# Kernel optimization log

Measured on AMD Instinct MI355X. Metric: run time of the kernel, lower is better.

The kernel has to match this reference:

```python
import jax, jax.numpy as jnp
import numpy as np

FREQ_MASK_PARAM = 20
TIME_MASK_PARAM = 40
NUM_FREQ_MASKS = 2
NUM_TIME_MASKS = 2
NOISE_STD = 0.01
P_APPLY = 0.5

B, C, F, T = 64, 2, 128, 2048


def setup_inputs() -> dict:
    key = jax.random.key(0)
    ks = jax.random.split(key, 7)
    return {
        "spec": jax.random.normal(ks[0], (B, C, F, T), dtype=jnp.float32),
        "apply_u": jax.random.uniform(ks[1], (B,), dtype=jnp.float32),
        "f_width_u": jax.random.uniform(ks[2], (B, NUM_FREQ_MASKS), dtype=jnp.float32),
        "f_start_u": jax.random.uniform(ks[3], (B, NUM_FREQ_MASKS), dtype=jnp.float32),
        "t_width_u": jax.random.uniform(ks[4], (B, NUM_TIME_MASKS), dtype=jnp.float32),
        "t_start_u": jax.random.uniform(ks[5], (B, NUM_TIME_MASKS), dtype=jnp.float32),
        "noise": jax.random.normal(ks[6], (B, C, F, T), dtype=jnp.float32),
    }


def _band_mask(width_u, start_u, size, max_param, clamp_min_one):
    # width = int(u * max_param); start = int(u * (size - width)) (optionally max(1, .))
    w = jnp.floor(width_u * max_param).astype(jnp.int32)          # [B, K]
    rng = (size - w).astype(jnp.float32)
    if clamp_min_one:
        rng = jnp.maximum(rng, 1.0)
    s0 = jnp.floor(start_u * rng).astype(jnp.int32)               # [B, K]
    idx = jnp.arange(size, dtype=jnp.int32)                       # [size]
    hit = (idx[None, None, :] >= s0[:, :, None]) & (idx[None, None, :] < (s0 + w)[:, :, None])
    return jnp.any(hit, axis=1)                                   # [B, size] True = zeroed


def reference(spec, apply_u, f_width_u, f_start_u, t_width_u, t_start_u, noise):
    b, c, f, t = spec.shape
    fmask = _band_mask(f_width_u, f_start_u, f, FREQ_MASK_PARAM, clamp_min_one=False)  # [B,F]
    tmask = _band_mask(t_width_u, t_start_u, t, TIME_MASK_PARAM, clamp_min_one=True)   # [B,T]
    keep = (~fmask)[:, None, :, None] & (~tmask)[:, None, None, :]                     # [B,1,F,T]
    aug = jnp.where(keep, spec, jnp.float32(0.0)) + noise * jnp.float32(NOISE_STD)
    apply = (apply_u <= P_APPLY)[:, None, None, None]
    return jnp.where(apply, aug, spec)
```

## Files before the change

kernel.cpp:

```cpp
#include <hip/hip_runtime.h>


#define BB 64
#define CC 2
#define FF 128
#define TT 2048

__global__ __launch_bounds__(256) void specaug_kernel(
    const float* __restrict__ spec,
    const float* __restrict__ apply_u,
    const float* __restrict__ f_width_u,
    const float* __restrict__ f_start_u,
    const float* __restrict__ t_width_u,
    const float* __restrict__ t_start_u,
    const float* __restrict__ noise,
    float* __restrict__ out)
{
    const int vec = blockIdx.x * blockDim.x + threadIdx.x;
    const int tv  = vec & (TT / 4 - 1);
    const int row = vec >> 9;
    const int f   = row & (FF - 1);
    const int b   = row >> 8;
    const int t0  = tv << 2;

    const float4 s = ((const float4*)spec)[vec];
    float4 o;

    if (apply_u[b] <= 0.5f) {
        bool fmask = false;
        #pragma unroll
        for (int k = 0; k < 2; ++k) {
            const int   w   = (int)floorf(f_width_u[b * 2 + k] * 20.0f);
            const float rng = (float)(FF - w);
            const int   s0  = (int)floorf(f_start_u[b * 2 + k] * rng);
            fmask |= (f >= s0) & (f < s0 + w);
        }
        int ts0[2], tw[2];
        #pragma unroll
        for (int k = 0; k < 2; ++k) {
            const int   w   = (int)floorf(t_width_u[b * 2 + k] * 40.0f);
            const float rng = fmaxf((float)(TT - w), 1.0f);
            ts0[k] = (int)floorf(t_start_u[b * 2 + k] * rng);
            tw[k]  = w;
        }

        const float4 n = ((const float4*)noise)[vec];
        const float sv[4] = {s.x, s.y, s.z, s.w};
        const float nv[4] = {n.x, n.y, n.z, n.w};
        float ov[4];
        #pragma unroll
        for (int j = 0; j < 4; ++j) {
            const int t = t0 + j;
            bool tmask = false;
            #pragma unroll
            for (int k = 0; k < 2; ++k)
                tmask |= (t >= ts0[k]) & (t < ts0[k] + tw[k]);
            const bool keep = (!fmask) & (!tmask);
            ov[j] = (keep ? sv[j] : 0.0f) + nv[j] * 0.01f;
        }
        o = make_float4(ov[0], ov[1], ov[2], ov[3]);
    } else {
        o = s;
    }
    ((float4*)out)[vec] = o;
}

extern "C" void kernel_launch(void* const* d_in, const int* in_sizes, int n_in,
                              void* d_out, int out_size, void* d_ws, size_t ws_size,
                              hipStream_t stream) {
    const float* spec      = (const float*)d_in[0];
    const float* apply_u   = (const float*)d_in[1];
    const float* f_width_u = (const float*)d_in[2];
    const float* f_start_u = (const float*)d_in[3];
    const float* t_width_u = (const float*)d_in[4];
    const float* t_start_u = (const float*)d_in[5];
    const float* noise     = (const float*)d_in[6];
    float* out             = (float*)d_out;

    const int total_vecs = BB * CC * FF * (TT / 4);
    const int block = 256;
    const int grid  = total_vecs / block;

    specaug_kernel<<<grid, block, 0, stream>>>(
        spec, apply_u, f_width_u, f_start_u, t_width_u, t_start_u, noise, out);
}
```

Baseline: 299.8 us.

## Process eight float4 vectors per thread with per-batch grid and nontemporal stores

Reorganizes the grid so each block row handles one batch and each thread handles eight strided float4 vectors, hoisting the mask parameter computation and time-mask evaluation out of the per-vector work. Stores use nontemporal hints to avoid cache pollution, and the non-applied batches take a pure copy path with batched loads. This aims to raise memory-level parallelism and cut redundant scalar work in a bandwidth-bound kernel, at the cost of fewer blocks and more registers per thread.

```diff
diff --git a/kernel.cpp b/kernel.cpp
--- a/kernel.cpp
+++ b/kernel.cpp
@@ -5,6 +5,12 @@
 #define CC 2
 #define FF 128
 #define TT 2048
+#define VB (CC * FF * (TT / 4))
+#define BLOCKS_X 64
+#define VPB 8
+#define STRIDE 16384
+
+typedef float f32x4 __attribute__((ext_vector_type(4)));
 
 __global__ __launch_bounds__(256) void specaug_kernel(
     const float* __restrict__ spec,
@@ -16,53 +22,63 @@
     const float* __restrict__ noise,
     float* __restrict__ out)
 {
-    const int vec = blockIdx.x * blockDim.x + threadIdx.x;
-    const int tv  = vec & (TT / 4 - 1);
-    const int row = vec >> 9;
-    const int f   = row & (FF - 1);
-    const int b   = row >> 8;
-    const int t0  = tv << 2;
+    const int b   = blockIdx.y;
+    const int tid = blockIdx.x * blockDim.x + threadIdx.x;
+    const int base = b * VB + tid;
 
-    const float4 s = ((const float4*)spec)[vec];
-    float4 o;
+    const f32x4* __restrict__ sp = (const f32x4*)spec;
+    const f32x4* __restrict__ np = (const f32x4*)noise;
+    f32x4* __restrict__ op = (f32x4*)out;
 
-    if (apply_u[b] <= 0.5f) {
-        bool fmask = false;
+    if (apply_u[b] > 0.5f) {
+        f32x4 v[VPB];
         #pragma unroll
-        for (int k = 0; k < 2; ++k) {
-            const int   w   = (int)floorf(f_width_u[b * 2 + k] * 20.0f);
-            const float rng = (float)(FF - w);
-            const int   s0  = (int)floorf(f_start_u[b * 2 + k] * rng);
-            fmask |= (f >= s0) & (f < s0 + w);
+        for (int j = 0; j < VPB; ++j) v[j] = sp[base + j * STRIDE];
+        #pragma unroll
+        for (int j = 0; j < VPB; ++j)
+            __builtin_nontemporal_store(v[j], &op[base + j * STRIDE]);
+        return;
+    }
+
+    int fs[2], fw[2], ts[2], tw[2];
+    #pragma unroll
+    for (int k = 0; k < 2; ++k) {
+        fw[k] = (int)floorf(f_width_u[b * 2 + k] * 20.0f);
+        fs[k] = (int)floorf(f_start_u[b * 2 + k] * (float)(FF - fw[k]));
+        tw[k] = (int)floorf(t_width_u[b * 2 + k] * 40.0f);
+        ts[k] = (int)floorf(t_start_u[b * 2 + k] *
+                            fmaxf((float)(TT - tw[k]), 1.0f));
+    }
+
+    const int t0 = (tid & (TT / 4 - 1)) << 2;
+    bool tm[4];
+    #pragma unroll
+    for (int jj = 0; jj < 4; ++jj) {
+        const int t = t0 + jj;
+        tm[jj] = ((t >= ts[0]) & (t < ts[0] + tw[0])) |
+                 ((t >= ts[1]) & (t < ts[1] + tw[1]));
+    }
+
+    f32x4 sv[VPB], nv[VPB];
+    #pragma unroll
+    for (int j = 0; j < VPB; ++j) sv[j] = sp[base + j * STRIDE];
+    #pragma unroll
+    for (int j = 0; j < VPB; ++j) nv[j] = np[base + j * STRIDE];
+
+    const int f0 = tid >> 9;
+    #pragma unroll
+    for (int j = 0; j < VPB; ++j) {
+        const int f = (f0 + 32 * j) & (FF - 1);
+        const bool fm = ((f >= fs[0]) & (f < fs[0] + fw[0])) |
+                        ((f >= fs[1]) & (f < fs[1] + fw[1]));
+        f32x4 o;
+        #pragma unroll
+        for (int jj = 0; jj < 4; ++jj) {
+            const bool keep = !(fm | tm[jj]);
+            o[jj] = (keep ? sv[j][jj] : 0.0f) + nv[j][jj] * 0.01f;
         }
-        int ts0[2], tw[2];
-        #pragma unroll
-        for (int k = 0; k < 2; ++k) {
-            const int   w   = (int)floorf(t_width_u[b * 2 + k] * 40.0f);
-            const float rng = fmaxf((float)(TT - w), 1.0f);
-            ts0[k] = (int)floorf(t_start_u[b * 2 + k] * rng);
-            tw[k]  = w;
-        }
-
-        const float4 n = ((const float4*)noise)[vec];
-        const float sv[4] = {s.x, s.y, s.z, s.w};
-        const float nv[4] = {n.x, n.y, n.z, n.w};
-        float ov[4];
-        #pragma unroll
-        for (int j = 0; j < 4; ++j) {
-            const int t = t0 + j;
-            bool tmask = false;
-            #pragma unroll
-            for (int k = 0; k < 2; ++k)
-                tmask |= (t >= ts0[k]) & (t < ts0[k] + tw[k]);
-            const bool keep = (!fmask) & (!tmask);
-            ov[j] = (keep ? sv[j] : 0.0f) + nv[j] * 0.01f;
-        }
-        o = make_float4(ov[0], ov[1], ov[2], ov[3]);
-    } else {
-        o = s;
+        __builtin_nontemporal_store(o, &op[base + j * STRIDE]);
     }
-    ((float4*)out)[vec] = o;
 }
 
 extern "C" void kernel_launch(void* const* d_in, const int* in_sizes, int n_in,
@@ -77,10 +93,7 @@
     const float* noise     = (const float*)d_in[6];
     float* out             = (float*)d_out;
 
-    const int total_vecs = BB * CC * FF * (TT / 4);
-    const int block = 256;
-    const int grid  = total_vecs / block;
-
-    specaug_kernel<<<grid, block, 0, stream>>>(
+    dim3 grid(BLOCKS_X, BB);
+    specaug_kernel<<<grid, 256, 0, stream>>>(
         spec, apply_u, f_width_u, f_start_u, t_width_u, t_start_u, noise, out);
 }
```

New measurement: 314.5 us. +4.9%, slower.
